# Optimization experiments

Measured on AMD Instinct MI355X. Metric: run time of the kernel, lower is better.

The kernel has to match this reference:

```python
import jax, jax.numpy as jnp
import numpy as np

D_MODEL = 1024
NUM_HEADS = 16
D_K = D_MODEL // NUM_HEADS
B, S = 1, 4096


def setup_inputs() -> dict:
    key = jax.random.key(0)
    ks = jax.random.split(key, 11)
    std = 1.0 / np.sqrt(D_MODEL)
    def lin(k):
        kw, kb = jax.random.split(k)
        W = jax.random.uniform(kw, (D_MODEL, D_MODEL), jnp.float32, -std, std)
        b = jax.random.uniform(kb, (D_MODEL,), jnp.float32, -std, std)
        return W, b
    Wq, bq = lin(ks[0]); Wk, bk = lin(ks[1]); Wv, bv = lin(ks[2]); Wo, bo = lin(ks[3])
    q = jax.random.normal(ks[4], (B, S, D_MODEL), jnp.float32)
    k = jax.random.normal(ks[5], (B, S, D_MODEL), jnp.float32)
    v = jax.random.normal(ks[6], (B, S, D_MODEL), jnp.float32)
    return {"q": q, "k": k, "v": v,
            "Wq": Wq, "bq": bq, "Wk": Wk, "bk": bk,
            "Wv": Wv, "bv": bv, "Wo": Wo, "bo": bo}


def reference(q, k, v, Wq, bq, Wk, bk, Wv, bv, Wo, bo):
    Bq, Sq, _ = q.shape
    # Linear projections (torch Linear: x @ W.T + b)
    def split_heads(x):
        return x.reshape(Bq, -1, NUM_HEADS, D_K).transpose(0, 2, 1, 3)  # [B,H,S,Dk]
    query = split_heads(q @ Wq.T + bq)
    key_ = split_heads(k @ Wk.T + bk)
    value = split_heads(v @ Wv.T + bv)
    scores = jnp.einsum('bhsd,bhtd->bhst', query, key_) / jnp.sqrt(jnp.float32(D_K))
    attn = jax.nn.softmax(scores, axis=-1)  # [B,H,S,S]
    ctx = jnp.einsum('bhst,bhtd->bhsd', attn, value)
    ctx = ctx.transpose(0, 2, 1, 3).reshape(Bq, Sq, NUM_HEADS * D_K)
    return ctx @ Wo.T + bo
```

## Files before the change

### kernel.cpp

```cpp
#include <hip/hip_runtime.h>
#include <cstdint>
#include <cstddef>

#define S_LEN 4096
#define DMODEL 1024
#define NHEADS 16
#define DK 64
#define ACT (S_LEN * DMODEL)
#define WELE (DMODEL * DMODEL)

typedef __bf16 bf16;
typedef bf16  bf16x2 __attribute__((ext_vector_type(2)));
typedef bf16  bf16x4 __attribute__((ext_vector_type(4)));
typedef bf16  bf16x8 __attribute__((ext_vector_type(8)));
typedef float f32x4  __attribute__((ext_vector_type(4)));
typedef float f32x16 __attribute__((ext_vector_type(16)));
typedef unsigned int uint32x4v __attribute__((ext_vector_type(4)));

__device__ __forceinline__ void async16(const void* g, void* l) {
    __builtin_amdgcn_global_load_lds(
        (__attribute__((address_space(1))) void*)(uintptr_t)g,
        (__attribute__((address_space(3))) void*)(uintptr_t)l,
        16, 0, 0);
}

__device__ __forceinline__ float fast_exp2(float x) {
#if __has_builtin(__builtin_amdgcn_exp2f)
    return __builtin_amdgcn_exp2f(x);
#else
    return exp2f(x);
#endif
}

__device__ __forceinline__ unsigned pk2(float a, float b) {
    bf16x2 t; t[0] = (bf16)a; t[1] = (bf16)b;
    return __builtin_bit_cast(unsigned, t);
}

__device__ __forceinline__ void pl32swap(unsigned &a, unsigned &b) {
    asm volatile("v_permlane32_swap_b32 %0, %1" : "+v"(a), "+v"(b));
}

__device__ __forceinline__ bf16x8 mkfrag(unsigned w0, unsigned w1, unsigned w2, unsigned w3) {
    uint32x4v u = { w0, w1, w2, w3 };
    return __builtin_bit_cast(bf16x8, u);
}

__global__ void __launch_bounds__(256) cvt7(
    const float* a0, const float* a1, const float* a2,
    const float* w0, const float* w1, const float* w2, const float* w3,
    bf16* oa0, bf16* oa1, bf16* oa2,
    bf16* ow0, bf16* ow1, bf16* ow2, bf16* ow3,
    int nA, int nB)
{
    const float* s; bf16* d; int n4;
    switch (blockIdx.y) {
        case 0: s = a0; d = oa0; n4 = nA; break;
        case 1: s = a1; d = oa1; n4 = nA; break;
        case 2: s = a2; d = oa2; n4 = nA; break;
        case 3: s = w0; d = ow0; n4 = nB; break;
        case 4: s = w1; d = ow1; n4 = nB; break;
        case 5: s = w2; d = ow2; n4 = nB; break;
        default: s = w3; d = ow3; n4 = nB; break;
    }
    int i = blockIdx.x * 256 + threadIdx.x;
    if (i < n4) {
        float4 v = ((const float4*)s)[i];
        bf16x4 r = { (bf16)v.x, (bf16)v.y, (bf16)v.z, (bf16)v.w };
        ((bf16x4*)d)[i] = r;
    }
}

__device__ __forceinline__ void gemm_compute_128(
    const bf16* As, const bf16* Bs, f32x4 (&acc)[4][4],
    int wm, int wn, int l16, int quad)
{
    bf16x8 af[4], bfr[4];
#pragma unroll
    for (int i = 0; i < 4; ++i)
        af[i] = *(const bf16x8*)&As[(wm + i * 16 + l16) * 32 + quad * 8];
#pragma unroll
    for (int i = 0; i < 4; ++i)
        bfr[i] = *(const bf16x8*)&Bs[(wn + i * 16 + l16) * 32 + quad * 8];
#pragma unroll
    for (int mi = 0; mi < 4; ++mi)
#pragma unroll
        for (int ni = 0; ni < 4; ++ni)
            acc[mi][ni] = __builtin_amdgcn_mfma_f32_16x16x32_bf16(
                af[mi], bfr[ni], acc[mi][ni], 0, 0, 0);
}

__device__ __forceinline__ void gemm_core_bk64(
    const bf16* __restrict__ A, const bf16* __restrict__ B,
    bf16* As, bf16* Bs, f32x4 (&acc)[4][4],
    int m0, int n0, int wm, int wn, int K)
{
    const int tid  = threadIdx.x;
    const int wave = tid >> 6;
    const int lane = tid & 63;
    const int quad = lane >> 4;
    const int l16  = lane & 15;

    const int srow = tid >> 2;
    const int scol = (tid & 3) * 8;
    const bf16* Ag = A + (size_t)(m0 + srow) * K + scol;
    const bf16* Bg = B + (size_t)(n0 + srow) * K + scol;
    char* lA = (char*)As + wave * 1024;
    char* lB = (char*)Bs + wave * 1024;

    for (int k0 = 0; k0 < K; k0 += 64) {
        async16(Ag,                       lA);
        async16(Ag + (size_t)64 * K,      lA + 4096);
        async16(Ag + 32,                  lA + 8192);
        async16(Ag + 32 + (size_t)64 * K, lA + 12288);
        async16(Bg,                       lB);
        async16(Bg + (size_t)64 * K,      lB + 4096);
        async16(Bg + 32,                  lB + 8192);
        async16(Bg + 32 + (size_t)64 * K, lB + 12288);
        Ag += 64; Bg += 64;
        __syncthreads();

        gemm_compute_128(As,        Bs,        acc, wm, wn, l16, quad);
        gemm_compute_128(As + 4096, Bs + 4096, acc, wm, wn, l16, quad);
        __syncthreads();
    }
}

__global__ void __launch_bounds__(256) proj_qkv(
    const bf16* __restrict__ Xq, const bf16* __restrict__ Wq, const float* __restrict__ bq, bf16* __restrict__ Qo,
    const bf16* __restrict__ Xk, const bf16* __restrict__ Wk, const float* __restrict__ bk, bf16* __restrict__ Ko,
    const bf16* __restrict__ Xv, const bf16* __restrict__ Wv, const float* __restrict__ bv, bf16* __restrict__ Vo,
    float qscale)
{
    __shared__ __align__(16) bf16 As[2 * 128 * 32];
    __shared__ __align__(16) bf16 Bs[2 * 128 * 32];

    const int which = blockIdx.z;
    const bf16*  A    = (which == 0) ? Xq : (which == 1) ? Xk : Xv;
    const bf16*  Bw   = (which == 0) ? Wq : (which == 1) ? Wk : Wv;
    const float* bias = (which == 0) ? bq : (which == 1) ? bk : bv;
    const float  scale = (which == 0) ? qscale : 1.0f;

    const int tid  = threadIdx.x;
    const int wave = tid >> 6;
    const int lane = tid & 63;
    const int quad = lane >> 4;
    const int l16  = lane & 15;
    const int m0 = blockIdx.x * 128;
    const int n0 = blockIdx.y * 128;
    const int wm = (wave & 1) * 64;
    const int wn = (wave >> 1) * 64;

    f32x4 acc[4][4] = {};
    gemm_core_bk64(A, Bw, As, Bs, acc, m0, n0, wm, wn, DMODEL);

    if (which < 2) {
        bf16* out = (which == 0) ? Qo : Ko;
#pragma unroll
        for (int mi = 0; mi < 4; ++mi)
#pragma unroll
            for (int ni = 0; ni < 4; ++ni) {
                const int n = n0 + wn + ni * 16 + l16;
                const float bn = bias[n];
                const int dk = n & 63;
                const int cc = dk >> 3, ee = dk & 7;
                const size_t hb = (size_t)(n >> 6) * S_LEN * DK;
#pragma unroll
                for (int r = 0; r < 4; ++r) {
                    const int m = m0 + wm + mi * 16 + quad * 4 + r;
                    const int pdk = ((cc ^ (m & 7)) << 3) | ee;
                    out[hb + (size_t)m * DK + pdk] = (bf16)((acc[mi][ni][r] + bn) * scale);
                }
            }
    } else {
#pragma unroll
        for (int mi = 0; mi < 4; ++mi)
#pragma unroll
            for (int ni = 0; ni < 4; ++ni) {
                const int n = n0 + wn + ni * 16 + l16;
                const float bn = bias[n];
                const int dk = n & 63;
                const size_t hb = (size_t)(n >> 6) * (64 * S_LEN);
                const int mbase = m0 + wm + mi * 16 + quad * 4;
                const int T  = mbase >> 6;
                const int tt = mbase & 63;
                const int pos = (((tt >> 3) ^ (dk & 7)) << 3) | (tt & 7);
                bf16x4 r4;
#pragma unroll
                for (int r = 0; r < 4; ++r) r4[r] = (bf16)(acc[mi][ni][r] + bn);
                *(bf16x4*)&Vo[hb + (size_t)T * 4096 + dk * 64 + pos] = r4;
            }
    }
}

__global__ void __launch_bounds__(256) gemm_out(
    const bf16* __restrict__ A, const bf16* __restrict__ Bw,
    const float* __restrict__ bias, float* __restrict__ out)
{
    __shared__ __align__(16) bf16 As[64 * 32];
    __shared__ __align__(16) bf16 Bs[128 * 32];

    const int tid  = threadIdx.x;
    const int wave = tid >> 6;
    const int lane = tid & 63;
    const int quad = lane >> 4;
    const int l16  = lane & 15;
    const int m0 = blockIdx.x * 64;
    const int n0 = blockIdx.y * 128;
    const int wm = (wave & 1) * 32;
    const int wn = (wave >> 1) * 64;

    const int srow = tid >> 2;
    const int scol = (tid & 3) * 8;
    const bf16* Ag  = A  + (size_t)(m0 + srow) * DMODEL + scol;
    const bf16* Bg  = Bw + (size_t)(n0 + srow) * DMODEL + scol;
    const bf16* Bg2 = Bg + (size_t)64 * DMODEL;

    f32x4 acc[2][4] = {};
    for (int k0 = 0; k0 < DMODEL; k0 += 32) {
        async16(Ag,  (char*)As + wave * 1024);
        async16(Bg,  (char*)Bs + wave * 1024);
        async16(Bg2, (char*)Bs + 4096 + wave * 1024);
        Ag += 32; Bg += 32; Bg2 += 32;
        __syncthreads();

        bf16x8 af[2], bfr[4];
#pragma unroll
        for (int i = 0; i < 2; ++i)
            af[i] = *(const bf16x8*)&As[(wm + i * 16 + l16) * 32 + quad * 8];
#pragma unroll
        for (int i = 0; i < 4; ++i)
            bfr[i] = *(const bf16x8*)&Bs[(wn + i * 16 + l16) * 32 + quad * 8];

#pragma unroll
        for (int mi = 0; mi < 2; ++mi)
#pragma unroll
            for (int ni = 0; ni < 4; ++ni)
                acc[mi][ni] = __builtin_amdgcn_mfma_f32_16x16x32_bf16(
                    af[mi], bfr[ni], acc[mi][ni], 0, 0, 0);
        __syncthreads();
    }

#pragma unroll
    for (int mi = 0; mi < 2; ++mi)
#pragma unroll
        for (int ni = 0; ni < 4; ++ni) {
            const int n = n0 + wn + ni * 16 + l16;
            const float bn = bias[n];
#pragma unroll
            for (int r = 0; r < 4; ++r) {
                const int m = m0 + wm + mi * 16 + quad * 4 + r;
                out[(size_t)m * DMODEL + n] = acc[mi][ni][r] + bn;
            }
        }
}

__global__ void __launch_bounds__(256, 2) flash_attn(
    const bf16* __restrict__ Q, const bf16* __restrict__ Kh,
    const bf16* __restrict__ Vt,
    float* __restrict__ O0, float* __restrict__ O1lo, float* __restrict__ O1hi,
    float* __restrict__ lsums)
{
    __shared__ __align__(16) bf16 Qs[256 * 64];
    __shared__ __align__(16) bf16 Ks[2][64 * 64];
    __shared__ __align__(16) bf16 Vs[2][64 * 64];

    const int tid  = threadIdx.x;
    const int wave = tid >> 6;
    const int lane = tid & 63;
    const int l31  = lane & 31;
    const int hi   = lane >> 5;
    const int x7   = lane & 7;
    const int s0 = blockIdx.x * 256;
    const int h  = blockIdx.y;
    const int z  = blockIdx.z;

    const bf16* Kg = Kh + (size_t)h * S_LEN * DK + (size_t)z * 2048 * DK + tid * 8;
    const bf16* Vg = Vt + (size_t)h * (64 * S_LEN) + (size_t)z * 32 * 4096 + tid * 8;

    {
        const bf16* Qg = Q + (size_t)h * S_LEN * DK + (size_t)s0 * DK + tid * 8;
#pragma unroll
        for (int j = 0; j < 8; ++j)
            async16(Qg + j * 2048, (char*)Qs + j * 4096 + wave * 1024);
    }
    async16(Kg,        (char*)Ks + wave * 1024);
    async16(Kg + 2048, (char*)Ks + 4096 + wave * 1024);
    async16(Vg,        (char*)Vs + wave * 1024);
    async16(Vg + 2048, (char*)Vs + 4096 + wave * 1024);
    Kg += 4096; Vg += 4096;
    __syncthreads();

    bf16x8 qf[2][4];
#pragma unroll
    for (int g = 0; g < 2; ++g) {
        const bf16* qb = &Qs[(wave * 64 + g * 32 + l31) * 64];
#pragma unroll
        for (int ks = 0; ks < 4; ++ks)
            qf[g][ks] = *(const bf16x8*)(qb + ((((ks << 1) + hi) ^ x7) << 3));
    }

    f32x16 od[2][2] = {};
    float lsum[2] = {};
    int cur = 0;

    for (int it = 0; it < 32; ++it) {
        if (it < 31) {
            char* lK = (char*)Ks + (cur ^ 1) * 8192 + wave * 1024;
            char* lV = (char*)Vs + (cur ^ 1) * 8192 + wave * 1024;
            async16(Kg,        lK);
            async16(Kg + 2048, lK + 4096);
            async16(Vg,        lV);
            async16(Vg + 2048, lV + 4096);
            Kg += 4096; Vg += 4096;
        }
        const bf16* Kc = &Ks[cur][0];
        const bf16* Vc = &Vs[cur][0];

        f32x16 st[2][2] = {};
        __builtin_amdgcn_s_setprio(1);
#pragma unroll
        for (int tt = 0; tt < 2; ++tt) {
            const bf16* kb = &Kc[(tt * 32 + l31) * 64];
#pragma unroll
            for (int ks = 0; ks < 4; ++ks) {
                bf16x8 kf = *(const bf16x8*)(kb + ((((ks << 1) + hi) ^ x7) << 3));
                st[0][tt] = __builtin_amdgcn_mfma_f32_32x32x16_bf16(kf, qf[0][ks], st[0][tt], 0, 0, 0);
                st[1][tt] = __builtin_amdgcn_mfma_f32_32x32x16_bf16(kf, qf[1][ks], st[1][tt], 0, 0, 0);
            }
        }
        __builtin_amdgcn_s_setprio(0);

        bf16x8 pf[2][4];
#pragma unroll
        for (int g = 0; g < 2; ++g)
#pragma unroll
            for (int tt = 0; tt < 2; ++tt) {
                float p[16];
#pragma unroll
                for (int r = 0; r < 16; ++r) {
                    p[r] = fast_exp2(st[g][tt][r]);
                    lsum[g] += p[r];
                }
#pragma unroll
                for (int w = 0; w < 2; ++w) {
                    const int G = w * 8;
                    unsigned A0 = pk2(p[G + 0], p[G + 1]);
                    unsigned A1 = pk2(p[G + 2], p[G + 3]);
                    unsigned B0 = pk2(p[G + 4], p[G + 5]);
                    unsigned B1 = pk2(p[G + 6], p[G + 7]);
                    pl32swap(A0, B0);
                    pl32swap(A1, B1);
                    pf[g][tt * 2 + w] = mkfrag(A0, A1, B0, B1);
                }
            }

        __builtin_amdgcn_s_setprio(1);
#pragma unroll
        for (int dd = 0; dd < 2; ++dd) {
            const bf16* vb = &Vc[(dd * 32 + l31) * 64];
#pragma unroll
            for (int ks = 0; ks < 4; ++ks) {
                bf16x8 vf = *(const bf16x8*)(vb + ((((ks << 1) + hi) ^ x7) << 3));
                od[0][dd] = __builtin_amdgcn_mfma_f32_32x32x16_bf16(vf, pf[0][ks], od[0][dd], 0, 0, 0);
                od[1][dd] = __builtin_amdgcn_mfma_f32_32x32x16_bf16(vf, pf[1][ks], od[1][dd], 0, 0, 0);
            }
        }
        __builtin_amdgcn_s_setprio(0);

        __syncthreads();
        cur ^= 1;
    }

    float* Ob = (z == 0) ? O0
              : (s0 < 2048 ? O1lo : O1hi - (size_t)2048 * DMODEL);
    float* lz = lsums + (size_t)z * S_LEN * NHEADS;
#pragma unroll
    for (int g = 0; g < 2; ++g) {
        float ls = lsum[g] + __shfl_xor(lsum[g], 32);
        const int s = s0 + wave * 64 + g * 32 + l31;
        if (hi == 0) lz[s * NHEADS + h] = ls;
        float* bp = Ob + (size_t)s * DMODEL + h * DK;
#pragma unroll
        for (int dd = 0; dd < 2; ++dd)
#pragma unroll
            for (int gg = 0; gg < 4; ++gg) {
                f32x4 r4 = { od[g][dd][gg * 4 + 0], od[g][dd][gg * 4 + 1],
                             od[g][dd][gg * 4 + 2], od[g][dd][gg * 4 + 3] };
                *(f32x4*)&bp[dd * 32 + gg * 8 + hi * 4] = r4;
            }
    }
}

__global__ void __launch_bounds__(256) combine(
    const float* __restrict__ O0, const float* __restrict__ O1lo,
    const float* __restrict__ O1hi, const float* __restrict__ lsums,
    bf16* __restrict__ ctxn)
{
    const int idx = blockIdx.x * 256 + threadIdx.x;
    const int s = idx >> 8;
    float4 a = ((const float4*)O0)[idx];
    float4 b = (s < 2048) ? ((const float4*)O1lo)[idx]
                          : ((const float4*)O1hi)[idx - 2048 * 256];
    const int sh = idx >> 4;
    const float rinv = 1.0f / (lsums[sh] + lsums[S_LEN * NHEADS + sh]);
    bf16x4 r = { (bf16)((a.x + b.x) * rinv), (bf16)((a.y + b.y) * rinv),
                 (bf16)((a.z + b.z) * rinv), (bf16)((a.w + b.w) * rinv) };
    ((bf16x4*)ctxn)[idx] = r;
}

extern "C" void kernel_launch(void* const* d_in, const int* in_sizes, int n_in,
                              void* d_out, int out_size, void* d_ws, size_t ws_size,
                              hipStream_t stream)
{
    (void)in_sizes; (void)n_in; (void)out_size; (void)ws_size;
    const float* q  = (const float*)d_in[0];
    const float* k  = (const float*)d_in[1];
    const float* v  = (const float*)d_in[2];
    const float* Wq = (const float*)d_in[3];
    const float* bq = (const float*)d_in[4];
    const float* Wk = (const float*)d_in[5];
    const float* bk = (const float*)d_in[6];
    const float* Wv = (const float*)d_in[7];
    const float* bv = (const float*)d_in[8];
    const float* Wo = (const float*)d_in[9];
    const float* bo = (const float*)d_in[10];

    bf16* Xq  = (bf16*)d_ws;
    bf16* Xk  = Xq  + ACT;
    bf16* Xv  = Xk  + ACT;
    bf16* Wqb = Xv  + ACT;
    bf16* Wkb = Wqb + WELE;
    bf16* Wvb = Wkb + WELE;
    bf16* Wob = Wvb + WELE;
    bf16* Qh  = Wob + WELE;
    bf16* Kh  = Qh  + ACT;
    bf16* Vt  = Kh  + ACT;
    bf16* CTX = Vt  + ACT;

    float* O0    = (float*)Xq;
    float* O1lo  = (float*)CTX;
    float* O1hi  = (float*)Xv;
    float* lsums = (float*)Wkb;
    bf16*  CTXn  = Qh;

    cvt7<<<dim3(ACT / 4 / 256, 7), 256, 0, stream>>>(
        q, k, v, Wq, Wk, Wv, Wo,
        Xq, Xk, Xv, Wqb, Wkb, Wvb, Wob, ACT / 4, WELE / 4);

    const float qscale = 0.125f * 1.4426950408889634f;
    proj_qkv<<<dim3(S_LEN / 128, DMODEL / 128, 3), 256, 0, stream>>>(
        Xq, Wqb, bq, Qh, Xk, Wkb, bk, Kh, Xv, Wvb, bv, Vt, qscale);

    flash_attn<<<dim3(S_LEN / 256, NHEADS, 2), 256, 0, stream>>>(
        Qh, Kh, Vt, O0, O1lo, O1hi, lsums);

    combine<<<dim3(ACT / 4 / 256), 256, 0, stream>>>(O0, O1lo, O1hi, lsums, CTXn);

    gemm_out<<<dim3(S_LEN / 64, DMODEL / 128), 256, 0, stream>>>(CTXn, Wob, bo, (float*)d_out);
}
```

Before: 256.1 us.

## Split attention KV into four chunks with bf16 partials and direct Q loads

```diff
diff --git a/kernel.cpp b/kernel.cpp
--- a/kernel.cpp
+++ b/kernel.cpp
@@ -255,13 +255,13 @@
         }
 }
 
-__global__ void __launch_bounds__(256, 2) flash_attn(
+__global__ void __launch_bounds__(256, 4) flash_attn(
     const bf16* __restrict__ Q, const bf16* __restrict__ Kh,
     const bf16* __restrict__ Vt,
-    float* __restrict__ O0, float* __restrict__ O1lo, float* __restrict__ O1hi,
+    bf16* __restrict__ Oz0, bf16* __restrict__ Oz1,
+    bf16* __restrict__ Oz2, bf16* __restrict__ Oz3,
     float* __restrict__ lsums)
 {
-    __shared__ __align__(16) bf16 Qs[256 * 64];
     __shared__ __align__(16) bf16 Ks[2][64 * 64];
     __shared__ __align__(16) bf16 Vs[2][64 * 64];
 
@@ -275,37 +275,32 @@
     const int h  = blockIdx.y;
     const int z  = blockIdx.z;
 
-    const bf16* Kg = Kh + (size_t)h * S_LEN * DK + (size_t)z * 2048 * DK + tid * 8;
-    const bf16* Vg = Vt + (size_t)h * (64 * S_LEN) + (size_t)z * 32 * 4096 + tid * 8;
-
-    {
-        const bf16* Qg = Q + (size_t)h * S_LEN * DK + (size_t)s0 * DK + tid * 8;
-#pragma unroll
-        for (int j = 0; j < 8; ++j)
-            async16(Qg + j * 2048, (char*)Qs + j * 4096 + wave * 1024);
-    }
+    const bf16* Kg = Kh + (size_t)h * S_LEN * DK + (size_t)z * 1024 * DK + tid * 8;
+    const bf16* Vg = Vt + (size_t)h * (64 * S_LEN) + (size_t)z * 16 * 4096 + tid * 8;
+
     async16(Kg,        (char*)Ks + wave * 1024);
     async16(Kg + 2048, (char*)Ks + 4096 + wave * 1024);
     async16(Vg,        (char*)Vs + wave * 1024);
     async16(Vg + 2048, (char*)Vs + 4096 + wave * 1024);
     Kg += 4096; Vg += 4096;
-    __syncthreads();
 
     bf16x8 qf[2][4];
 #pragma unroll
     for (int g = 0; g < 2; ++g) {
-        const bf16* qb = &Qs[(wave * 64 + g * 32 + l31) * 64];
+        const bf16* qb = Q + (size_t)h * S_LEN * DK
+                           + (size_t)(s0 + wave * 64 + g * 32 + l31) * DK;
 #pragma unroll
         for (int ks = 0; ks < 4; ++ks)
             qf[g][ks] = *(const bf16x8*)(qb + ((((ks << 1) + hi) ^ x7) << 3));
     }
+    __syncthreads();
 
     f32x16 od[2][2] = {};
     float lsum[2] = {};
     int cur = 0;
 
-    for (int it = 0; it < 32; ++it) {
-        if (it < 31) {
+    for (int it = 0; it < 16; ++it) {
+        if (it < 15) {
             char* lK = (char*)Ks + (cur ^ 1) * 8192 + wave * 1024;
             char* lV = (char*)Vs + (cur ^ 1) * 8192 + wave * 1024;
             async16(Kg,        lK);
@@ -372,41 +367,44 @@
         cur ^= 1;
     }
 
-    float* Ob = (z == 0) ? O0
-              : (s0 < 2048 ? O1lo : O1hi - (size_t)2048 * DMODEL);
+    bf16* Ob = (z == 0) ? Oz0 : (z == 1) ? Oz1 : (z == 2) ? Oz2 : Oz3;
     float* lz = lsums + (size_t)z * S_LEN * NHEADS;
 #pragma unroll
     for (int g = 0; g < 2; ++g) {
         float ls = lsum[g] + __shfl_xor(lsum[g], 32);
         const int s = s0 + wave * 64 + g * 32 + l31;
         if (hi == 0) lz[s * NHEADS + h] = ls;
-        float* bp = Ob + (size_t)s * DMODEL + h * DK;
+        bf16* bp = Ob + (size_t)s * DMODEL + h * DK;
 #pragma unroll
         for (int dd = 0; dd < 2; ++dd)
 #pragma unroll
             for (int gg = 0; gg < 4; ++gg) {
-                f32x4 r4 = { od[g][dd][gg * 4 + 0], od[g][dd][gg * 4 + 1],
-                             od[g][dd][gg * 4 + 2], od[g][dd][gg * 4 + 3] };
-                *(f32x4*)&bp[dd * 32 + gg * 8 + hi * 4] = r4;
+                bf16x4 r4 = { (bf16)od[g][dd][gg * 4 + 0], (bf16)od[g][dd][gg * 4 + 1],
+                              (bf16)od[g][dd][gg * 4 + 2], (bf16)od[g][dd][gg * 4 + 3] };
+                *(bf16x4*)&bp[dd * 32 + gg * 8 + hi * 4] = r4;
             }
     }
 }
 
 __global__ void __launch_bounds__(256) combine(
-    const float* __restrict__ O0, const float* __restrict__ O1lo,
-    const float* __restrict__ O1hi, const float* __restrict__ lsums,
-    bf16* __restrict__ ctxn)
+    const bf16* __restrict__ Oz0, const bf16* __restrict__ Oz1,
+    const bf16* __restrict__ Oz2, const bf16* __restrict__ Oz3,
+    const float* __restrict__ lsums, bf16* __restrict__ ctxn)
 {
     const int idx = blockIdx.x * 256 + threadIdx.x;
-    const int s = idx >> 8;
-    float4 a = ((const float4*)O0)[idx];
-    float4 b = (s < 2048) ? ((const float4*)O1lo)[idx]
-                          : ((const float4*)O1hi)[idx - 2048 * 256];
-    const int sh = idx >> 4;
-    const float rinv = 1.0f / (lsums[sh] + lsums[S_LEN * NHEADS + sh]);
-    bf16x4 r = { (bf16)((a.x + b.x) * rinv), (bf16)((a.y + b.y) * rinv),
-                 (bf16)((a.z + b.z) * rinv), (bf16)((a.w + b.w) * rinv) };
-    ((bf16x4*)ctxn)[idx] = r;
+    const int sh = idx >> 3;
+    const int SH = S_LEN * NHEADS;
+    const float rinv = 1.0f / (lsums[sh] + lsums[SH + sh] +
+                               lsums[2 * SH + sh] + lsums[3 * SH + sh]);
+    bf16x8 a = ((const bf16x8*)Oz0)[idx];
+    bf16x8 b = ((const bf16x8*)Oz1)[idx];
+    bf16x8 c = ((const bf16x8*)Oz2)[idx];
+    bf16x8 d = ((const bf16x8*)Oz3)[idx];
+    bf16x8 r;
+#pragma unroll
+    for (int j = 0; j < 8; ++j)
+        r[j] = (bf16)(((float)a[j] + (float)b[j] + (float)c[j] + (float)d[j]) * rinv);
+    ((bf16x8*)ctxn)[idx] = r;
 }
 
 extern "C" void kernel_launch(void* const* d_in, const int* in_sizes, int n_in,
@@ -438,10 +436,11 @@
     bf16* Vt  = Kh  + ACT;
     bf16* CTX = Vt  + ACT;
 
-    float* O0    = (float*)Xq;
-    float* O1lo  = (float*)CTX;
-    float* O1hi  = (float*)Xv;
-    float* lsums = (float*)Wkb;
+    bf16*  Oz0   = Xq;
+    bf16*  Oz1   = Xk;
+    bf16*  Oz2   = Xv;
+    bf16*  Oz3   = CTX;
+    float* lsums = (float*)Wqb;
     bf16*  CTXn  = Qh;
 
     cvt7<<<dim3(ACT / 4 / 256, 7), 256, 0, stream>>>(
@@ -452,10 +451,11 @@
     proj_qkv<<<dim3(S_LEN / 128, DMODEL / 128, 3), 256, 0, stream>>>(
         Xq, Wqb, bq, Qh, Xk, Wkb, bk, Kh, Xv, Wvb, bv, Vt, qscale);
 
-    flash_attn<<<dim3(S_LEN / 256, NHEADS, 2), 256, 0, stream>>>(
-        Qh, Kh, Vt, O0, O1lo, O1hi, lsums);
-
-    combine<<<dim3(ACT / 4 / 256), 256, 0, stream>>>(O0, O1lo, O1hi, lsums, CTXn);
+    flash_attn<<<dim3(S_LEN / 256, NHEADS, 4), 256, 0, stream>>>(
+        Qh, Kh, Vt, Oz0, Oz1, Oz2, Oz3, lsums);
+
+    combine<<<dim3(ACT / 8 / 256), 256, 0, stream>>>(
+        Oz0, Oz1, Oz2, Oz3, lsums, CTXn);
 
     gemm_out<<<dim3(S_LEN / 64, DMODEL / 128), 256, 0, stream>>>(CTXn, Wob, bo, (float*)d_out);
 }
```

Result: slower. 647.9 us (+153.0%).
